# Kernel optimization log

Hardware: AMD Instinct MI355X
Metric: run time of the kernel (lower is better)

## Reference

```python
import jax, jax.numpy as jnp
import numpy as np

D = 1024   # d_model
E = 8      # num_experts
K = 2      # top-k routes per token
B = 8192   # tokens (== max_tokens)
CAP = 1280 # ceil(1.25 * 8192 / 8)


def setup_inputs() -> dict:
    key = jax.random.key(0)
    ks = jax.random.split(key, 11)
    s = 1.0 / np.sqrt(D)
    u = lambda k_, shp: jax.random.uniform(k_, shp, jnp.float32, -s, s)
    return {
        "x": jax.random.normal(ks[0], (B, D), jnp.float32),
        "W1": u(ks[1], (E, D, D)),
        "b1": u(ks[2], (E, D)),
        "W2": u(ks[3], (E, D, D)),
        "b2": u(ks[4], (E, D)),
        "Wf1": u(ks[5], (D, D)),
        "bf1": u(ks[6], (D,)),
        "Wf2": u(ks[7], (D, D)),
        "bf2": u(ks[8], (D,)),
        "routes": jax.random.randint(ks[9], (B, K), 0, E, jnp.int32),
        "capacity": CAP,
    }


def reference(x, W1, b1, W2, b2, Wf1, bf1, Wf2, bf2, routes, capacity):
    Bn, Dm = x.shape
    En = W1.shape[0]
    Kk = routes.shape[1]

    # --- capacity-aware acceptance (vectorized equivalent of the sequential loop) ---
    # A (token,slot) assignment to expert e is accepted iff the number of earlier
    # valid assignments to e (flattened token-major, slot-minor order) is < capacity.
    # This is exactly the torch loop semantics: load only grows on accept, and once
    # it hits capacity every later assignment to that expert is rejected.
    e = routes.reshape(-1)                                   # [B*K]
    valid = (e >= 0) & (e < En)
    e_safe = jnp.where(valid, e, 0)
    oh = jax.nn.one_hot(e_safe, En, dtype=jnp.int32) * valid[:, None].astype(jnp.int32)
    rank = jnp.cumsum(oh, axis=0) - oh                        # exclusive prefix count [B*K, E]
    rank_at = jnp.take_along_axis(rank, e_safe[:, None], axis=1)[:, 0]
    accept = (valid & (rank_at < capacity)).reshape(Bn, Kk)   # [B, K]

    # --- dense per-expert 2-layer MLP (grouped GEMM form) ---
    # torch Linear: y = x @ W.T + b, W is [out, in]
    h = jax.nn.relu(jnp.einsum('bd,ehd->ebh', x, W1) + b1[:, None, :])  # [E,B,D]
    y = jnp.einsum('ebh,eoh->ebo', h, W2) + b2[:, None, :]              # [E,B,D]

    # --- combine accepted expert outputs per token ---
    yt = jnp.transpose(y, (1, 0, 2))                          # [B,E,D]
    idx = e_safe.reshape(Bn, Kk)
    g = jnp.take_along_axis(yt, idx[:, :, None], axis=1)      # [B,K,D]
    af = accept.astype(x.dtype)
    summed = jnp.sum(af[:, :, None] * g, axis=1)              # [B,D]
    used = jnp.sum(af, axis=1)                                # [B]

    # --- fallback MLP for overflowed tokens ---
    fb = jax.nn.relu(x @ Wf1.T + bf1) @ Wf2.T + bf2

    out = jnp.where((used > 0)[:, None], summed / jnp.maximum(used, 1.0)[:, None], fb)
    return out
```

## Files before the change

### kernel.cpp

```cpp
#include <hip/hip_runtime.h>

#define DM    1024
#define NEXP  8
#define BTOK  8192
#define KTOP  2
#define NASSIGN (BTOK*KTOP)
#define CAPC  1280
#define MROWS (NEXP*CAPC)

#define MTILES_E (MROWS/128)
#define MTILES_F (BTOK/128)
#define NTILES   (DM/128)
#define SLOTS_E  (10*NTILES)
#define SLOTS_F  (MTILES_F*NTILES/8)
#define SLOTS    (SLOTS_E+SLOTS_F)
#define GRID_L   (8*SLOTS)

typedef unsigned short ushort_t;
typedef __attribute__((ext_vector_type(8))) __bf16 bf16x8;
typedef __attribute__((ext_vector_type(4))) float  f32x4;

__device__ __forceinline__ ushort_t f2b(float f) {
  union { float f; unsigned u; } a; a.f = f;
  unsigned u = a.u;
  return (ushort_t)((u + 0x7FFFu + ((u >> 16) & 1u)) >> 16);
}
__device__ __forceinline__ float b2f(ushort_t h) {
  union { unsigned u; float f; } a; a.u = ((unsigned)h) << 16;
  return a.f;
}

#define GLOAD_LDS(g, l) __builtin_amdgcn_global_load_lds( \
    (const __attribute__((address_space(1))) void*)(g),   \
    (__attribute__((address_space(3))) void*)(l), 16, 0, 0)

__global__ void route_cvt_kernel(const int* __restrict__ routes, const int* __restrict__ capp,
                                 int* __restrict__ gidx, int* __restrict__ slot,
                                 int* __restrict__ counts, int* __restrict__ nfb,
                                 const float* __restrict__ W1, const float* __restrict__ W2,
                                 const float* __restrict__ Wf1, const float* __restrict__ Wf2,
                                 ushort_t* __restrict__ o1, ushort_t* __restrict__ o2,
                                 ushort_t* __restrict__ of1, ushort_t* __restrict__ of2) {
  const int b = blockIdx.x, t = threadIdx.x;
  if (b >= 8) {
    const float* s; ushort_t* d; int idx;
    int c = b - 8;
    if (c < 2048)      { s = W1;  d = o1;  idx = c; }
    else if (c < 4096) { s = W2;  d = o2;  idx = c - 2048; }
    else if (c < 4352) { s = Wf1; d = of1; idx = c - 4096; }
    else               { s = Wf2; d = of2; idx = c - 4352; }
    int i = idx * 1024 + t;
    float4 v = ((const float4*)s)[i];
    ushort4 o; o.x = f2b(v.x); o.y = f2b(v.y); o.z = f2b(v.z); o.w = f2b(v.w);
    ((ushort4*)d)[i] = o;
    return;
  }
  const int e = b;
  const int lane = t & 63, w = t >> 6;
  int cap = *capp; if (cap > CAPC) cap = CAPC;
  if (e == 0 && t == 0) *nfb = 0;
  __shared__ int wtot[16];
  int base = 0;
  for (int i0 = 0; i0 < NASSIGN; i0 += 1024) {
    int i = i0 + t;
    int r = routes[i];
    bool mine = (r == e);
    unsigned long long mask = __ballot(mine);
    int pre = __popcll(mask & ((1ull << lane) - 1ull));
    if (lane == 0) wtot[w] = __popcll(mask);
    __syncthreads();
    int tot = 0;
#pragma unroll
    for (int j = 0; j < 16; ++j) { int c = wtot[j]; if (j < w) pre += c; tot += c; }
    if (e == 0 && (unsigned)r >= NEXP) slot[i] = -1;
    if (mine) {
      int pos = base + pre;
      if (pos < cap) { gidx[e * CAPC + pos] = i >> 1; slot[i] = e * CAPC + pos; }
      else slot[i] = -1;
    }
    base += tot;
    __syncthreads();
  }
  if (t == 0) counts[e] = base < cap ? base : cap;
}

__global__ void fblist_gxg_kernel(const int* __restrict__ slot, int* __restrict__ fbidx,
                                  int* __restrict__ nfb,
                                  const float* __restrict__ x, const int* __restrict__ gidx,
                                  const int* __restrict__ counts, ushort_t* __restrict__ xg) {
  int b = blockIdx.x, t = threadIdx.x;
  if (b < 32) {
    int tok = b * 256 + t;
    int u = (slot[2 * tok] >= 0) + (slot[2 * tok + 1] >= 0);
    if (u == 0) { int p = atomicAdd(nfb, 1); fbidx[p] = tok; }
    return;
  }
  int row = b - 32;
  int e = row / CAPC, p = row % CAPC;
  int d = t * 4;
  ushort4 o = {0, 0, 0, 0};
  if (p < counts[e]) {
    int tok = gidx[row];
    float4 v = *(const float4*)(x + (size_t)tok * DM + d);
    o.x = f2b(v.x); o.y = f2b(v.y); o.z = f2b(v.z); o.w = f2b(v.w);
  }
  *(ushort4*)(xg + (size_t)row * DM + d) = o;
}

__global__ void gather_xf_kernel(const float* __restrict__ x, const int* __restrict__ fbidx,
                                 const int* __restrict__ nfbp, ushort_t* __restrict__ xf) {
  int row = blockIdx.x;
  int n = *nfbp;
  int nr = (n + 127) & ~127;
  if (row >= nr) return;
  int d = threadIdx.x * 4;
  ushort4 o = {0, 0, 0, 0};
  if (row < n) {
    int tok = fbidx[row];
    float4 v = *(const float4*)(x + (size_t)tok * DM + d);
    o.x = f2b(v.x); o.y = f2b(v.y); o.z = f2b(v.z); o.w = f2b(v.w);
  }
  *(ushort4*)(xf + (size_t)row * DM + d) = o;
}

template <int RELU, int FBSCAT>
__global__ __launch_bounds__(256, 4) void layer_kernel(
    const ushort_t* __restrict__ Ae, const ushort_t* __restrict__ We,
    const float* __restrict__ be, ushort_t* __restrict__ Ce,
    const ushort_t* __restrict__ Af, const ushort_t* __restrict__ Wf,
    const float* __restrict__ bfp, ushort_t* __restrict__ Cf,
    float* __restrict__ outF, const int* __restrict__ scat,
    const int* __restrict__ nfbp) {
  const int b = blockIdx.x;
  const int xcd = b & 7, s = b >> 3;
  const ushort_t* A; const ushort_t* W; const float* bias; ushort_t* C;
  int mgrp, ntile; bool isfb;
  if (s < SLOTS_E) {
    const int e = xcd;
    mgrp = e * 10 + (s >> 3); ntile = s & 7;
    A = Ae; W = We + (size_t)e * DM * DM; bias = be + e * DM; C = Ce; isfb = false;
  } else {
    int fl = (s - SLOTS_E) * 8 + xcd;
    mgrp = fl >> 3; ntile = fl & 7;
    if (mgrp * 128 >= *nfbp) return;
    A = Af; W = Wf; bias = bfp; C = Cf; isfb = true;
  }
  const int tid = threadIdx.x, lane = tid & 63, w = tid >> 6;
  const int wr = w >> 1, wc = w & 1;
  __shared__ ushort_t smem[16384];
  const size_t Abase = (size_t)mgrp * 128 * DM;
  const size_t Wbase = (size_t)ntile * 128 * DM;
  f32x4 acc[4][4] = {};

  const int sub  = lane >> 2;
  const int slt  = lane & 3;
  const int gcol = (slt ^ ((sub >> 1) & 3)) * 8;
  const int r0 = (w * 2)     * 16 + sub;
  const int r1 = (w * 2 + 1) * 16 + sub;

#define STAGE(T, BUF) do { int kt_ = (T) * 32; int ao_ = (BUF) * 4096;          \
    GLOAD_LDS(A + Abase + (size_t)r0 * DM + kt_ + gcol, smem + ao_ + (w*2)  *512); \
    GLOAD_LDS(A + Abase + (size_t)r1 * DM + kt_ + gcol, smem + ao_ + (w*2+1)*512); \
    GLOAD_LDS(W + Wbase + (size_t)r0 * DM + kt_ + gcol, smem + 8192 + ao_ + (w*2)  *512); \
    GLOAD_LDS(W + Wbase + (size_t)r1 * DM + kt_ + gcol, smem + 8192 + ao_ + (w*2+1)*512); \
  } while (0)

  const int fr    = lane & 15, g = lane >> 4;
  const int rslot = (g ^ ((fr >> 1) & 3)) * 8;

  STAGE(0, 0);
  for (int t = 0; t < 32; ++t) {
    __syncthreads();
    if (t + 1 < 32) STAGE(t + 1, (t + 1) & 1);
    const ushort_t* bA = smem + (t & 1) * 4096;
    const ushort_t* bB = smem + 8192 + (t & 1) * 4096;
    bf16x8 av[4], bv[4];
#pragma unroll
    for (int m = 0; m < 4; ++m)
      av[m] = *(const bf16x8*)&bA[(wr * 64 + m * 16 + fr) * 32 + rslot];
#pragma unroll
    for (int n = 0; n < 4; ++n)
      bv[n] = *(const bf16x8*)&bB[(wc * 64 + n * 16 + fr) * 32 + rslot];
#pragma unroll
    for (int m = 0; m < 4; ++m)
#pragma unroll
      for (int n = 0; n < 4; ++n)
        acc[m][n] = __builtin_amdgcn_mfma_f32_16x16x32_bf16(av[m], bv[n], acc[m][n], 0, 0, 0);
  }
#undef STAGE

  if (FBSCAT && isfb) {
    int nfbv = *nfbp;
#pragma unroll
    for (int n = 0; n < 4; ++n) {
      int col = ntile * 128 + wc * 64 + n * 16 + fr;
      float bb = bias[col];
#pragma unroll
      for (int m = 0; m < 4; ++m) {
        int row0 = mgrp * 128 + wr * 64 + m * 16 + g * 4;
#pragma unroll
        for (int r = 0; r < 4; ++r) {
          int row = row0 + r;
          if (row < nfbv) outF[(size_t)scat[row] * DM + col] = acc[m][n][r] + bb;
        }
      }
    }
  } else {
    __syncthreads();
#pragma unroll
    for (int n = 0; n < 4; ++n) {
      int col = wc * 64 + n * 16 + fr;
      float bb = bias[ntile * 128 + col];
#pragma unroll
      for (int m = 0; m < 4; ++m) {
        int lrow0 = wr * 64 + m * 16 + g * 4;
#pragma unroll
        for (int r = 0; r < 4; ++r) {
          float v = acc[m][n][r] + bb;
          if (RELU) v = v > 0.0f ? v : 0.0f;
          smem[(lrow0 + r) * 128 + col] = f2b(v);
        }
      }
    }
    __syncthreads();
    ushort_t* Cb = C + (size_t)mgrp * 128 * DM + ntile * 128;
#pragma unroll
    for (int q = 0; q < 8; ++q) {
      int chunk = q * 256 + tid;
      int row = chunk >> 4, co = (chunk & 15) * 8;
      bf16x8 v = *(const bf16x8*)&smem[row * 128 + co];
      *(bf16x8*)(Cb + (size_t)row * DM + co) = v;
    }
  }
}

__global__ void combine_kernel(const ushort_t* __restrict__ Y, const int* __restrict__ slot,
                               float* __restrict__ out) {
  int t = blockIdx.x;
  int s0 = slot[2 * t], s1 = slot[2 * t + 1];
  int u = (s0 >= 0) + (s1 >= 0);
  if (u == 0) return;
  int d = threadIdx.x * 4;
  float a0 = 0, a1 = 0, a2 = 0, a3 = 0;
  if (s0 >= 0) {
    ushort4 q = *(const ushort4*)(Y + (size_t)s0 * DM + d);
    a0 += b2f(q.x); a1 += b2f(q.y); a2 += b2f(q.z); a3 += b2f(q.w);
  }
  if (s1 >= 0) {
    ushort4 q = *(const ushort4*)(Y + (size_t)s1 * DM + d);
    a0 += b2f(q.x); a1 += b2f(q.y); a2 += b2f(q.z); a3 += b2f(q.w);
  }
  float inv = 1.0f / (float)u;
  float4 o = make_float4(a0 * inv, a1 * inv, a2 * inv, a3 * inv);
  *(float4*)(out + (size_t)t * DM + d) = o;
}

extern "C" void kernel_launch(void* const* d_in, const int* in_sizes, int n_in,
                              void* d_out, int out_size, void* d_ws, size_t ws_size,
                              hipStream_t stream) {
  const float* x   = (const float*)d_in[0];
  const float* W1  = (const float*)d_in[1];
  const float* b1  = (const float*)d_in[2];
  const float* W2  = (const float*)d_in[3];
  const float* b2  = (const float*)d_in[4];
  const float* Wf1 = (const float*)d_in[5];
  const float* bf1 = (const float*)d_in[6];
  const float* Wf2 = (const float*)d_in[7];
  const float* bf2 = (const float*)d_in[8];
  const int* routes = (const int*)d_in[9];
  const int* capp   = (const int*)d_in[10];
  float* out = (float*)d_out;

  char* ws = (char*)d_ws;
  size_t off = 0;
  auto alloc = [&](size_t bytes) -> void* {
    void* p = ws + off; off += (bytes + 255) & ~255ull; return p;
  };
  ushort_t* W1b  = (ushort_t*)alloc((size_t)NEXP * DM * DM * 2);
  ushort_t* W2b  = (ushort_t*)alloc((size_t)NEXP * DM * DM * 2);
  ushort_t* Wf1b = (ushort_t*)alloc((size_t)DM * DM * 2);
  ushort_t* Wf2b = (ushort_t*)alloc((size_t)DM * DM * 2);
  ushort_t* xg   = (ushort_t*)alloc((size_t)MROWS * DM * 2);
  ushort_t* H    = (ushort_t*)alloc((size_t)MROWS * DM * 2);
  ushort_t* Y    = (ushort_t*)alloc((size_t)MROWS * DM * 2);
  ushort_t* xf   = (ushort_t*)alloc((size_t)BTOK * DM * 2);
  ushort_t* Hf   = (ushort_t*)alloc((size_t)BTOK * DM * 2);
  int* gidx   = (int*)alloc(MROWS * 4);
  int* slot   = (int*)alloc(NASSIGN * 4);
  int* counts = (int*)alloc(NEXP * 4);
  int* fbidx  = (int*)alloc(BTOK * 4);
  int* nfb    = (int*)alloc(4);

  route_cvt_kernel<<<8 + 4608, 1024, 0, stream>>>(routes, capp, gidx, slot, counts, nfb,
                                                  W1, W2, Wf1, Wf2, W1b, W2b, Wf1b, Wf2b);
  fblist_gxg_kernel<<<32 + MROWS, 256, 0, stream>>>(slot, fbidx, nfb, x, gidx, counts, xg);
  gather_xf_kernel<<<BTOK, 256, 0, stream>>>(x, fbidx, nfb, xf);
  layer_kernel<1, 0><<<GRID_L, 256, 0, stream>>>(xg, W1b, b1, H, xf, Wf1b, bf1, Hf,
                                                 nullptr, nullptr, nfb);
  layer_kernel<0, 1><<<GRID_L, 256, 0, stream>>>(H, W2b, b2, Y, Hf, Wf2b, bf2, nullptr,
                                                 out, fbidx, nfb);
  combine_kernel<<<BTOK, 256, 0, stream>>>(Y, slot, out);
}
```

Baseline: 140.3 us.

## Enlarge GEMM tiles to 256x256 with 8 waves and finer-grained software pipeline

The grouped GEMM layer kernel moves from 128x128 tiles with 4 waves to 256x256 tiles with 8 waves and 128 KB of LDS. The K loop is now split into half-steps with interleaved global-to-LDS prefetches, explicit s_barrier/waitcnt control and s_setprio around MFMA bursts. The goal is to double operand reuse per byte loaded and to overlap loads with MFMA. In exchange the grid shrinks sharply (288 blocks), occupancy is lower, and the hand-tuned barrier/waitcnt schedule is fragile.

```diff
diff --git a/kernel.cpp b/kernel.cpp
--- a/kernel.cpp
+++ b/kernel.cpp
@@ -8,11 +8,8 @@
 #define CAPC  1280
 #define MROWS (NEXP*CAPC)
 
-#define MTILES_E (MROWS/128)
-#define MTILES_F (BTOK/128)
-#define NTILES   (DM/128)
-#define SLOTS_E  (10*NTILES)
-#define SLOTS_F  (MTILES_F*NTILES/8)
+#define SLOTS_E  20
+#define SLOTS_F  16
 #define SLOTS    (SLOTS_E+SLOTS_F)
 #define GRID_L   (8*SLOTS)
 
@@ -123,8 +120,11 @@
   *(ushort4*)(xf + (size_t)row * DM + d) = o;
 }
 
+#define BAR() do { asm volatile("s_barrier" ::: "memory"); \
+                   __builtin_amdgcn_sched_barrier(0); } while (0)
+
 template <int RELU, int FBSCAT>
-__global__ __launch_bounds__(256, 4) void layer_kernel(
+__global__ __launch_bounds__(512, 2) void layer_kernel(
     const ushort_t* __restrict__ Ae, const ushort_t* __restrict__ We,
     const float* __restrict__ be, ushort_t* __restrict__ Ce,
     const ushort_t* __restrict__ Af, const ushort_t* __restrict__ Wf,
@@ -137,67 +137,102 @@
   int mgrp, ntile; bool isfb;
   if (s < SLOTS_E) {
     const int e = xcd;
-    mgrp = e * 10 + (s >> 3); ntile = s & 7;
+    mgrp = e * 5 + (s >> 2); ntile = s & 3;
     A = Ae; W = We + (size_t)e * DM * DM; bias = be + e * DM; C = Ce; isfb = false;
   } else {
     int fl = (s - SLOTS_E) * 8 + xcd;
-    mgrp = fl >> 3; ntile = fl & 7;
-    if (mgrp * 128 >= *nfbp) return;
+    mgrp = fl >> 2; ntile = fl & 3;
+    if (mgrp * 256 >= *nfbp) return;
     A = Af; W = Wf; bias = bfp; C = Cf; isfb = true;
   }
   const int tid = threadIdx.x, lane = tid & 63, w = tid >> 6;
-  const int wr = w >> 1, wc = w & 1;
-  __shared__ ushort_t smem[16384];
-  const size_t Abase = (size_t)mgrp * 128 * DM;
-  const size_t Wbase = (size_t)ntile * 128 * DM;
-  f32x4 acc[4][4] = {};
+  const int wr = w >> 2, wc = w & 3;
+  __shared__ ushort_t smem[65536];
+  const size_t Abase = (size_t)mgrp * 256 * DM;
+  const size_t Wbase = (size_t)ntile * 256 * DM;
+  f32x4 acc[8][4] = {};
 
   const int sub  = lane >> 2;
   const int slt  = lane & 3;
   const int gcol = (slt ^ ((sub >> 1) & 3)) * 8;
-  const int r0 = (w * 2)     * 16 + sub;
-  const int r1 = (w * 2 + 1) * 16 + sub;
-
-#define STAGE(T, BUF) do { int kt_ = (T) * 32; int ao_ = (BUF) * 4096;          \
-    GLOAD_LDS(A + Abase + (size_t)r0 * DM + kt_ + gcol, smem + ao_ + (w*2)  *512); \
-    GLOAD_LDS(A + Abase + (size_t)r1 * DM + kt_ + gcol, smem + ao_ + (w*2+1)*512); \
-    GLOAD_LDS(W + Wbase + (size_t)r0 * DM + kt_ + gcol, smem + 8192 + ao_ + (w*2)  *512); \
-    GLOAD_LDS(W + Wbase + (size_t)r1 * DM + kt_ + gcol, smem + 8192 + ao_ + (w*2+1)*512); \
+#define ALB(BUF, KH) ((BUF)*16384 + (KH)*8192)
+#define BLB(BUF, KH) (32768 + (BUF)*16384 + (KH)*8192)
+#define STAGEH(P, GB, T, KH, LB) do { int kt_ = (T)*64 + (KH)*32;                    \
+    GLOAD_LDS(P + GB + (size_t)((w*2  )*16 + sub)*DM + kt_ + gcol, smem + (LB) + (w*2  )*512); \
+    GLOAD_LDS(P + GB + (size_t)((w*2+1)*16 + sub)*DM + kt_ + gcol, smem + (LB) + (w*2+1)*512); \
   } while (0)
 
-  const int fr    = lane & 15, g = lane >> 4;
+  const int fr = lane & 15, g = lane >> 4;
   const int rslot = (g ^ ((fr >> 1) & 3)) * 8;
-
-  STAGE(0, 0);
-  for (int t = 0; t < 32; ++t) {
-    __syncthreads();
-    if (t + 1 < 32) STAGE(t + 1, (t + 1) & 1);
-    const ushort_t* bA = smem + (t & 1) * 4096;
-    const ushort_t* bB = smem + 8192 + (t & 1) * 4096;
-    bf16x8 av[4], bv[4];
-#pragma unroll
-    for (int m = 0; m < 4; ++m)
-      av[m] = *(const bf16x8*)&bA[(wr * 64 + m * 16 + fr) * 32 + rslot];
-#pragma unroll
-    for (int n = 0; n < 4; ++n)
-      bv[n] = *(const bf16x8*)&bB[(wc * 64 + n * 16 + fr) * 32 + rslot];
-#pragma unroll
-    for (int m = 0; m < 4; ++m)
-#pragma unroll
-      for (int n = 0; n < 4; ++n)
-        acc[m][n] = __builtin_amdgcn_mfma_f32_16x16x32_bf16(av[m], bv[n], acc[m][n], 0, 0, 0);
-  }
-#undef STAGE
+  bf16x8 av[4], bv[4];
+#define LOADFRAGS(BUF, MH, KH) do {                                                  \
+    const ushort_t* pa_ = smem + ALB(BUF, KH);                                       \
+    const ushort_t* pb_ = smem + BLB(BUF, KH);                                       \
+    _Pragma("unroll")                                                                \
+    for (int i_ = 0; i_ < 4; ++i_)                                                   \
+      av[i_] = *(const bf16x8*)&pa_[(wr*128 + ((MH)*4 + i_)*16 + fr)*32 + rslot];    \
+    _Pragma("unroll")                                                                \
+    for (int n_ = 0; n_ < 4; ++n_)                                                   \
+      bv[n_] = *(const bf16x8*)&pb_[(wc*64 + n_*16 + fr)*32 + rslot];                \
+  } while (0)
+#define DOMFMA(MH) do { __builtin_amdgcn_s_setprio(1);                               \
+    _Pragma("unroll")                                                                \
+    for (int i_ = 0; i_ < 4; ++i_)                                                   \
+      _Pragma("unroll")                                                              \
+      for (int n_ = 0; n_ < 4; ++n_)                                                 \
+        acc[(MH)*4 + i_][n_] = __builtin_amdgcn_mfma_f32_16x16x32_bf16(              \
+            av[i_], bv[n_], acc[(MH)*4 + i_][n_], 0, 0, 0);                          \
+    __builtin_amdgcn_s_setprio(0); } while (0)
+#define VM2() do { asm volatile("s_waitcnt vmcnt(2)" ::: "memory");                  \
+                   __builtin_amdgcn_sched_barrier(0); } while (0)
+
+  STAGEH(A, Abase, 0, 0, ALB(0,0));  STAGEH(W, Wbase, 0, 0, BLB(0,0));
+  STAGEH(A, Abase, 0, 1, ALB(0,1));  STAGEH(W, Wbase, 0, 1, BLB(0,1));
+  STAGEH(A, Abase, 1, 0, ALB(1,0));  STAGEH(W, Wbase, 1, 0, BLB(1,0));
+  asm volatile("s_waitcnt vmcnt(4)" ::: "memory");
+  BAR();
+
+  for (int j = 0; j < 8; ++j) {
+    const int bT = 2*j + 1, cT = (2*j + 2) & 15, dT = (2*j + 3) & 15;
+    LOADFRAGS(0, 0, 0);
+    STAGEH(W, Wbase, bT, 1, BLB(1,1));
+    BAR(); DOMFMA(0); BAR();
+    LOADFRAGS(0, 1, 0);
+    STAGEH(A, Abase, bT, 1, ALB(1,1));
+    BAR(); DOMFMA(1); BAR();
+    LOADFRAGS(0, 0, 1);
+    STAGEH(A, Abase, cT, 0, ALB(0,0));
+    BAR(); DOMFMA(0); BAR();
+    VM2();
+    LOADFRAGS(0, 1, 1);
+    STAGEH(W, Wbase, cT, 0, BLB(0,0));
+    BAR(); DOMFMA(1); BAR();
+    LOADFRAGS(1, 0, 0);
+    STAGEH(A, Abase, cT, 1, ALB(0,1));
+    STAGEH(W, Wbase, cT, 1, BLB(0,1));
+    BAR(); DOMFMA(0); BAR();
+    LOADFRAGS(1, 1, 0);
+    BAR(); DOMFMA(1); BAR();
+    LOADFRAGS(1, 0, 1);
+    STAGEH(A, Abase, dT, 0, ALB(1,0));
+    BAR(); DOMFMA(0); BAR();
+    VM2();
+    LOADFRAGS(1, 1, 1);
+    STAGEH(W, Wbase, dT, 0, BLB(1,0));
+    BAR(); DOMFMA(1); BAR();
+  }
+  asm volatile("s_waitcnt vmcnt(0)" ::: "memory");
+  BAR();
 
   if (FBSCAT && isfb) {
     int nfbv = *nfbp;
 #pragma unroll
     for (int n = 0; n < 4; ++n) {
-      int col = ntile * 128 + wc * 64 + n * 16 + fr;
+      int col = ntile * 256 + wc * 64 + n * 16 + fr;
       float bb = bias[col];
 #pragma unroll
-      for (int m = 0; m < 4; ++m) {
-        int row0 = mgrp * 128 + wr * 64 + m * 16 + g * 4;
+      for (int m = 0; m < 8; ++m) {
+        int row0 = mgrp * 256 + wr * 128 + m * 16 + g * 4;
 #pragma unroll
         for (int r = 0; r < 4; ++r) {
           int row = row0 + r;
@@ -206,29 +241,28 @@
       }
     }
   } else {
-    __syncthreads();
 #pragma unroll
     for (int n = 0; n < 4; ++n) {
       int col = wc * 64 + n * 16 + fr;
-      float bb = bias[ntile * 128 + col];
-#pragma unroll
-      for (int m = 0; m < 4; ++m) {
-        int lrow0 = wr * 64 + m * 16 + g * 4;
+      float bb = bias[ntile * 256 + col];
+#pragma unroll
+      for (int m = 0; m < 8; ++m) {
+        int lrow0 = wr * 128 + m * 16 + g * 4;
 #pragma unroll
         for (int r = 0; r < 4; ++r) {
           float v = acc[m][n][r] + bb;
           if (RELU) v = v > 0.0f ? v : 0.0f;
-          smem[(lrow0 + r) * 128 + col] = f2b(v);
+          smem[(lrow0 + r) * 256 + col] = f2b(v);
         }
       }
     }
     __syncthreads();
-    ushort_t* Cb = C + (size_t)mgrp * 128 * DM + ntile * 128;
-#pragma unroll
-    for (int q = 0; q < 8; ++q) {
-      int chunk = q * 256 + tid;
-      int row = chunk >> 4, co = (chunk & 15) * 8;
-      bf16x8 v = *(const bf16x8*)&smem[row * 128 + co];
+    ushort_t* Cb = C + (size_t)mgrp * 256 * DM + ntile * 256;
+#pragma unroll
+    for (int q = 0; q < 16; ++q) {
+      int chunk = q * 512 + tid;
+      int row = chunk >> 5, co = (chunk & 31) * 8;
+      bf16x8 v = *(const bf16x8*)&smem[row * 256 + co];
       *(bf16x8*)(Cb + (size_t)row * DM + co) = v;
     }
   }
@@ -295,9 +329,9 @@
                                                   W1, W2, Wf1, Wf2, W1b, W2b, Wf1b, Wf2b);
   fblist_gxg_kernel<<<32 + MROWS, 256, 0, stream>>>(slot, fbidx, nfb, x, gidx, counts, xg);
   gather_xf_kernel<<<BTOK, 256, 0, stream>>>(x, fbidx, nfb, xf);
-  layer_kernel<1, 0><<<GRID_L, 256, 0, stream>>>(xg, W1b, b1, H, xf, Wf1b, bf1, Hf,
+  layer_kernel<1, 0><<<GRID_L, 512, 0, stream>>>(xg, W1b, b1, H, xf, Wf1b, bf1, Hf,
                                                  nullptr, nullptr, nfb);
-  layer_kernel<0, 1><<<GRID_L, 256, 0, stream>>>(H, W2b, b2, Y, Hf, Wf2b, bf2, nullptr,
+  layer_kernel<0, 1><<<GRID_L, 512, 0, stream>>>(H, W2b, b2, Y, Hf, Wf2b, bf2, nullptr,
                                                  out, fbidx, nfb);
   combine_kernel<<<BTOK, 256, 0, stream>>>(Y, slot, out);
 }
```

Result: faster. 135.5 us (-3.4%).
